# Kernel optimization log

Measured on AMD Instinct MI355X. Metric: run time of the kernel, lower is better.

## Reference

```python
import jax, jax.numpy as jnp
import numpy as np


def setup_inputs() -> dict:
    key = jax.random.key(0)
    k1, k2 = jax.random.split(key)
    inputs = jax.random.normal(k1, (32, 4096, 64), dtype=jnp.float32)
    embed = jax.random.normal(k2, (64, 1024), dtype=jnp.float32)  # [embed_dim, n_embed]
    return {"inputs": inputs, "embed": embed}


def reference(inputs, embed):
    # Eval-mode forward of VectorQuantizer (self.training == False, no EMA update).
    embed_dim, n_embed = embed.shape
    flat = inputs.reshape(-1, embed_dim)  # [N, D]
    # distances[n, k] = ||flat_n||^2 - 2 flat_n . e_k + ||e_k||^2
    distances = (
        jnp.sum(flat * flat, axis=1, keepdims=True)
        - 2.0 * (flat @ embed)
        + jnp.sum(embed * embed, axis=0, keepdims=True)
    )  # [N, n_embed]
    # torch.argmax(-distances, 1) == argmin(distances, 1) (same first-occurrence tie-break)
    encoding_indices = jnp.argmin(distances, axis=1)  # [N] int
    idx = encoding_indices.reshape(inputs.shape[:-1])  # [B, T]
    # quantize: F.embedding(idx, embed.T) -> gather rows of embed.T
    quantized = jnp.take(embed.T, idx, axis=0)  # [B, T, D]
    codes = jnp.concatenate([inputs, quantized], axis=-1)  # [B, T, 2D]
    # straight-through estimator
    quantized_st = inputs + jax.lax.stop_gradient(quantized - inputs)
    return quantized_st, codes, idx
```

## Files before the change

### kernel.cpp

```cpp
#include <hip/hip_runtime.h>

#define D 64
#define KCODES 1024
#define PTS_PER_BLK 256
#define MTILES 16
#define NT 4
#define CODE_CHUNKS 4
#define PTILES 512
#define WL_CAP 2048

typedef _Float16 f16x8 __attribute__((ext_vector_type(8)));
typedef float f32x4 __attribute__((ext_vector_type(4)));

static __device__ __forceinline__ unsigned short f2h(float f) {
  _Float16 h = (_Float16)f;
  return __builtin_bit_cast(unsigned short, h);
}

static __device__ __forceinline__ void evalExact(const float* __restrict__ inputs,
                                                 const float* __restrict__ embedT,
                                                 const float* __restrict__ en2,
                                                 const float* s_fn2,
                                                 int p0blk, int pl, int c,
                                                 unsigned long long* s_best) {
  int p = p0blk + pl;
  const float* f = inputs + (size_t)p * D;
  const float* e = embedT + (size_t)c * D;
  float a0 = 0.f, a1 = 0.f, a2 = 0.f, a3 = 0.f;
#pragma unroll
  for (int d = 0; d < D; d += 4) {
    a0 = fmaf(f[d + 0], e[d + 0], a0);
    a1 = fmaf(f[d + 1], e[d + 1], a1);
    a2 = fmaf(f[d + 2], e[d + 2], a2);
    a3 = fmaf(f[d + 3], e[d + 3], a3);
  }
  float dot = (a0 + a1) + (a2 + a3);
  float dist = fmaf(-2.f, dot, s_fn2[pl]) + en2[c];
  unsigned long long key = ((unsigned long long)__float_as_uint(dist) << 32) | (unsigned)c;
  atomicMin(&s_best[pl], key);
}

__global__ void __launch_bounds__(256) vq_prep(const float* __restrict__ embed,
                                               const float* __restrict__ inputs,
                                               float* __restrict__ embedT,
                                               unsigned short* __restrict__ embedTh,
                                               float* __restrict__ en2,
                                               int* __restrict__ en2max_bits,
                                               float* __restrict__ fn2,
                                               unsigned long long* __restrict__ best) {
  const int bid = blockIdx.x;
  const int tid = threadIdx.x;
  if (bid < KCODES / 256) {
    int k = bid * 256 + tid;
    float row[D];
    float s = 0.f;
#pragma unroll
    for (int d = 0; d < D; ++d) {
      float e = embed[d * KCODES + k];
      row[d] = e;
      s = fmaf(e, e, s);
    }
    en2[k] = s;
    float4* o4 = reinterpret_cast<float4*>(embedT + (size_t)k * D);
#pragma unroll
    for (int j = 0; j < 16; ++j)
      o4[j] = make_float4(row[4 * j], row[4 * j + 1], row[4 * j + 2], row[4 * j + 3]);
    unsigned us[32];
#pragma unroll
    for (int j = 0; j < 32; ++j) {
      unsigned lo = f2h(row[2 * j]);
      unsigned hi = f2h(row[2 * j + 1]);
      us[j] = lo | (hi << 16);
    }
    uint4* ob = reinterpret_cast<uint4*>(embedTh + (size_t)k * D);
#pragma unroll
    for (int j = 0; j < 8; ++j)
      ob[j] = make_uint4(us[4 * j], us[4 * j + 1], us[4 * j + 2], us[4 * j + 3]);
    float m = s;
#pragma unroll
    for (int off = 32; off; off >>= 1) m = fmaxf(m, __shfl_down(m, off, 64));
    if ((tid & 63) == 0) atomicMax(en2max_bits, __float_as_int(m));
  } else {
    int p = (bid - KCODES / 256) * 256 + tid;
    const float4* i4 = reinterpret_cast<const float4*>(inputs + (size_t)p * D);
    float s = 0.f;
#pragma unroll
    for (int j = 0; j < 16; ++j) {
      float4 v = i4[j];
      s = fmaf(v.x, v.x, s); s = fmaf(v.y, v.y, s);
      s = fmaf(v.z, v.z, s); s = fmaf(v.w, v.w, s);
    }
    fn2[p] = s;
    best[p] = ~0ull;
  }
}

__global__ void __launch_bounds__(256, 4) vq_partial(
    const float* __restrict__ inputs, const float* __restrict__ embedT,
    const unsigned short* __restrict__ embedTh, const float* __restrict__ en2,
    const float* __restrict__ fn2, const int* __restrict__ en2max_bits,
    unsigned long long* __restrict__ best) {
  __shared__ unsigned long long s_best[PTS_PER_BLK];
  __shared__ unsigned s_wl[WL_CAP];
  __shared__ int s_wcount;
  __shared__ float s_fn2[PTS_PER_BLK];
  __shared__ float s_wmin[2][4][16];

  const int tid = threadIdx.x;
  const int w = tid >> 6;
  const int l = tid & 63;
  const int l15 = l & 15;
  const int lg = l >> 4;
  const int chunk = blockIdx.x / PTILES;
  const int ptile = blockIdx.x % PTILES;
  const int p0blk = ptile * PTS_PER_BLK;
  const int cb = chunk * 256 + w * 64;

  s_best[tid] = ~0ull;
  if (tid == 0) s_wcount = 0;
  s_fn2[tid] = fn2[p0blk + tid];

  const float en2max = __int_as_float(*en2max_bits);

  f16x8 bfr[NT][2];
  float en2v[NT];
#pragma unroll
  for (int t = 0; t < NT; ++t) {
    const f16x8* bp = reinterpret_cast<const f16x8*>(
        embedTh + (size_t)(cb + 16 * t + l15) * D + lg * 8);
    bfr[t][0] = bp[0];
    bfr[t][1] = bp[4];
    en2v[t] = en2[cb + 16 * t + l15];
  }

  __syncthreads();

#pragma unroll 1
  for (int mt = 0; mt < MTILES; ++mt) {
    const int p0 = p0blk + mt * 16;
    const float* arow = inputs + (size_t)(p0 + l15) * D + lg * 8;
    float4 a0 = *reinterpret_cast<const float4*>(arow + 0);
    float4 a1 = *reinterpret_cast<const float4*>(arow + 4);
    float4 a2 = *reinterpret_cast<const float4*>(arow + 32);
    float4 a3 = *reinterpret_cast<const float4*>(arow + 36);
    f16x8 af0, af1;
    af0[0] = (_Float16)a0.x; af0[1] = (_Float16)a0.y; af0[2] = (_Float16)a0.z; af0[3] = (_Float16)a0.w;
    af0[4] = (_Float16)a1.x; af0[5] = (_Float16)a1.y; af0[6] = (_Float16)a1.z; af0[7] = (_Float16)a1.w;
    af1[0] = (_Float16)a2.x; af1[1] = (_Float16)a2.y; af1[2] = (_Float16)a2.z; af1[3] = (_Float16)a2.w;
    af1[4] = (_Float16)a3.x; af1[5] = (_Float16)a3.y; af1[6] = (_Float16)a3.z; af1[7] = (_Float16)a3.w;

    f32x4 acc[NT];
#pragma unroll
    for (int t = 0; t < NT; ++t) acc[t] = (f32x4){0.f, 0.f, 0.f, 0.f};
#pragma unroll
    for (int t = 0; t < NT; ++t)
      acc[t] = __builtin_amdgcn_mfma_f32_16x16x32_f16(af0, bfr[t][0], acc[t], 0, 0, 0);
#pragma unroll
    for (int t = 0; t < NT; ++t)
      acc[t] = __builtin_amdgcn_mfma_f32_16x16x32_f16(af1, bfr[t][1], acc[t], 0, 0, 0);

#pragma unroll
    for (int t = 0; t < NT; ++t)
#pragma unroll
      for (int r = 0; r < 4; ++r)
        acc[t][r] = fmaf(-2.f, acc[t][r], en2v[t]);

    float m[4];
#pragma unroll
    for (int r = 0; r < 4; ++r) {
      float mm = acc[0][r];
#pragma unroll
      for (int t = 1; t < NT; ++t) mm = fminf(mm, acc[t][r]);
#pragma unroll
      for (int s = 1; s < 16; s <<= 1) mm = fminf(mm, __shfl_xor(mm, s, 16));
      m[r] = mm;
    }
    if (l15 == 0) {
#pragma unroll
      for (int r = 0; r < 4; ++r) s_wmin[mt & 1][w][lg * 4 + r] = m[r];
    }
    __syncthreads();
    float fnv[4];
#pragma unroll
    for (int r = 0; r < 4; ++r) fnv[r] = s_fn2[mt * 16 + lg * 4 + r];
    float thr[4];
#pragma unroll
    for (int r = 0; r < 4; ++r) {
      int q = lg * 4 + r;
      float fm = fminf(fminf(s_wmin[mt & 1][0][q], s_wmin[mt & 1][1][q]),
                       fminf(s_wmin[mt & 1][2][q], s_wmin[mt & 1][3][q]));
      thr[r] = fm + (0.00390625f * sqrtf(fnv[r] * en2max) + 0.01f);
    }
#pragma unroll
    for (int t = 0; t < NT; ++t)
#pragma unroll
      for (int r = 0; r < 4; ++r)
        if (acc[t][r] <= thr[r]) {
          int pl = mt * 16 + lg * 4 + r;
          int c = cb + 16 * t + l15;
          int pos = atomicAdd(&s_wcount, 1);
          if (pos < WL_CAP) s_wl[pos] = (unsigned)((pl << 10) | c);
          else evalExact(inputs, embedT, en2, s_fn2, p0blk, pl, c, s_best);
        }
  }

  __syncthreads();

  int wc = s_wcount; if (wc > WL_CAP) wc = WL_CAP;
  for (int i = tid; i < wc; i += 256)
    evalExact(inputs, embedT, en2, s_fn2, p0blk, (int)(s_wl[i] >> 10), (int)(s_wl[i] & 1023), s_best);
  __syncthreads();

  atomicMin(&best[p0blk + tid], s_best[tid]);
}

__global__ void __launch_bounds__(256) vq_finalize(
    const float* __restrict__ inputs, const float* __restrict__ embedT,
    const unsigned long long* __restrict__ best,
    float* __restrict__ out_q, float* __restrict__ out_codes,
    float* __restrict__ out_idx) {
  const int tid = threadIdx.x;
  const int p0blk = blockIdx.x * 256;
  const int sub = tid & 3;
#pragma unroll 1
  for (int pass = 0; pass < 4; ++pass) {
    int pl = pass * 64 + (tid >> 2);
    int p = p0blk + pl;
    unsigned long long key = best[p];
    int c = (int)(unsigned)(key & 0xFFFFFFFFu);
    const f32x4* qrow = reinterpret_cast<const f32x4*>(embedT + (size_t)c * D);
    const f32x4* frow = reinterpret_cast<const f32x4*>(inputs + (size_t)p * D);
    f32x4* oq = reinterpret_cast<f32x4*>(out_q + (size_t)p * D);
    f32x4* oc = reinterpret_cast<f32x4*>(out_codes + (size_t)p * 2 * D);
#pragma unroll
    for (int j = 0; j < 4; ++j) {
      int i4 = j * 4 + sub;
      f32x4 qv = qrow[i4];
      f32x4 fv = frow[i4];
      oq[i4] = qv;
      oc[i4] = fv;
      oc[16 + i4] = qv;
    }
    if (sub == 0) out_idx[p] = (float)c;
  }
}

extern "C" void kernel_launch(void* const* d_in, const int* in_sizes, int n_in,
                              void* d_out, int out_size, void* d_ws, size_t ws_size,
                              hipStream_t stream) {
  const float* inputs = (const float*)d_in[0];
  const float* embed  = (const float*)d_in[1];
  int N = in_sizes[0] / D;

  unsigned long long* best  = (unsigned long long*)d_ws;
  float* embedT             = (float*)(best + N);
  unsigned short* embedTh   = (unsigned short*)(embedT + KCODES * D);
  float* en2                = (float*)(embedTh + KCODES * D);
  float* fn2                = en2 + KCODES;
  int* en2max_bits          = (int*)(fn2 + N);

  float* out = (float*)d_out;
  float* out_q     = out;
  float* out_codes = out + (size_t)N * D;
  float* out_idx   = out + (size_t)N * D * 3;

  vq_prep<<<KCODES / 256 + N / 256, 256, 0, stream>>>(embed, inputs, embedT, embedTh,
                                                      en2, en2max_bits, fn2, best);
  vq_partial<<<CODE_CHUNKS * PTILES, 256, 0, stream>>>(inputs, embedT, embedTh, en2,
                                                       fn2, en2max_bits, best);
  vq_finalize<<<N / 256, 256, 0, stream>>>(inputs, embedT, best, out_q, out_codes, out_idx);
}
```

Before: 314.4 us.

## Drop per-tile block barrier via wave-local thresholds and deferred refinement; prefetch next A tile

Candidate filtering no longer waits on a block-wide barrier every M-tile. Each wave now filters against its own local minimum plus margin. Candidates are stored together with their approximate distance, and after the loop they are re-filtered against the block-wide threshold before exact evaluation. The input rows for the next tile are also loaded one iteration ahead to hide global load latency. The trade-offs are a larger shared worklist (64-bit entries), more candidates collected because wave-local thresholds are looser, and a higher chance of overflowing the worklist, which triggers inline exact evaluation.

New measurement: 379.9 us. 1.21x slower.

```diff
diff --git a/kernel.cpp b/kernel.cpp
--- a/kernel.cpp
+++ b/kernel.cpp
@@ -101,10 +101,11 @@
     const float* __restrict__ fn2, const int* __restrict__ en2max_bits,
     unsigned long long* __restrict__ best) {
   __shared__ unsigned long long s_best[PTS_PER_BLK];
-  __shared__ unsigned s_wl[WL_CAP];
+  __shared__ unsigned long long s_wl[WL_CAP];
   __shared__ int s_wcount;
   __shared__ float s_fn2[PTS_PER_BLK];
-  __shared__ float s_wmin[2][4][16];
+  __shared__ float s_pmin[4][PTS_PER_BLK];
+  __shared__ float s_thr[PTS_PER_BLK];
 
   const int tid = threadIdx.x;
   const int w = tid >> 6;
@@ -135,19 +136,29 @@
 
   __syncthreads();
 
+  float4 A0, A1, A2, A3;
+  {
+    const float* arow = inputs + (size_t)(p0blk + l15) * D + lg * 8;
+    A0 = *reinterpret_cast<const float4*>(arow + 0);
+    A1 = *reinterpret_cast<const float4*>(arow + 4);
+    A2 = *reinterpret_cast<const float4*>(arow + 32);
+    A3 = *reinterpret_cast<const float4*>(arow + 36);
+  }
+
 #pragma unroll 1
   for (int mt = 0; mt < MTILES; ++mt) {
-    const int p0 = p0blk + mt * 16;
-    const float* arow = inputs + (size_t)(p0 + l15) * D + lg * 8;
-    float4 a0 = *reinterpret_cast<const float4*>(arow + 0);
-    float4 a1 = *reinterpret_cast<const float4*>(arow + 4);
-    float4 a2 = *reinterpret_cast<const float4*>(arow + 32);
-    float4 a3 = *reinterpret_cast<const float4*>(arow + 36);
+    const int mtn = (mt + 1 < MTILES) ? mt + 1 : mt;
+    const float* an = inputs + (size_t)(p0blk + mtn * 16 + l15) * D + lg * 8;
+    float4 N0 = *reinterpret_cast<const float4*>(an + 0);
+    float4 N1 = *reinterpret_cast<const float4*>(an + 4);
+    float4 N2 = *reinterpret_cast<const float4*>(an + 32);
+    float4 N3 = *reinterpret_cast<const float4*>(an + 36);
+
     f16x8 af0, af1;
-    af0[0] = (_Float16)a0.x; af0[1] = (_Float16)a0.y; af0[2] = (_Float16)a0.z; af0[3] = (_Float16)a0.w;
-    af0[4] = (_Float16)a1.x; af0[5] = (_Float16)a1.y; af0[6] = (_Float16)a1.z; af0[7] = (_Float16)a1.w;
-    af1[0] = (_Float16)a2.x; af1[1] = (_Float16)a2.y; af1[2] = (_Float16)a2.z; af1[3] = (_Float16)a2.w;
-    af1[4] = (_Float16)a3.x; af1[5] = (_Float16)a3.y; af1[6] = (_Float16)a3.z; af1[7] = (_Float16)a3.w;
+    af0[0] = (_Float16)A0.x; af0[1] = (_Float16)A0.y; af0[2] = (_Float16)A0.z; af0[3] = (_Float16)A0.w;
+    af0[4] = (_Float16)A1.x; af0[5] = (_Float16)A1.y; af0[6] = (_Float16)A1.z; af0[7] = (_Float16)A1.w;
+    af1[0] = (_Float16)A2.x; af1[1] = (_Float16)A2.y; af1[2] = (_Float16)A2.z; af1[3] = (_Float16)A2.w;
+    af1[4] = (_Float16)A3.x; af1[5] = (_Float16)A3.y; af1[6] = (_Float16)A3.z; af1[7] = (_Float16)A3.w;
 
     f32x4 acc[NT];
 #pragma unroll
@@ -177,38 +188,50 @@
     }
     if (l15 == 0) {
 #pragma unroll
-      for (int r = 0; r < 4; ++r) s_wmin[mt & 1][w][lg * 4 + r] = m[r];
-    }
-    __syncthreads();
-    float fnv[4];
-#pragma unroll
-    for (int r = 0; r < 4; ++r) fnv[r] = s_fn2[mt * 16 + lg * 4 + r];
-    float thr[4];
+      for (int r = 0; r < 4; ++r) s_pmin[w][mt * 16 + lg * 4 + r] = m[r];
+    }
+    float fnv[4], thrw[4];
 #pragma unroll
     for (int r = 0; r < 4; ++r) {
-      int q = lg * 4 + r;
-      float fm = fminf(fminf(s_wmin[mt & 1][0][q], s_wmin[mt & 1][1][q]),
-                       fminf(s_wmin[mt & 1][2][q], s_wmin[mt & 1][3][q]));
-      thr[r] = fm + (0.00390625f * sqrtf(fnv[r] * en2max) + 0.01f);
+      fnv[r] = s_fn2[mt * 16 + lg * 4 + r];
+      thrw[r] = m[r] + (0.00390625f * sqrtf(fnv[r] * en2max) + 0.01f);
     }
 #pragma unroll
     for (int t = 0; t < NT; ++t)
 #pragma unroll
       for (int r = 0; r < 4; ++r)
-        if (acc[t][r] <= thr[r]) {
+        if (acc[t][r] <= thrw[r]) {
           int pl = mt * 16 + lg * 4 + r;
           int c = cb + 16 * t + l15;
           int pos = atomicAdd(&s_wcount, 1);
-          if (pos < WL_CAP) s_wl[pos] = (unsigned)((pl << 10) | c);
-          else evalExact(inputs, embedT, en2, s_fn2, p0blk, pl, c, s_best);
+          if (pos < WL_CAP)
+            s_wl[pos] = ((unsigned long long)__float_as_uint(acc[t][r]) << 32) |
+                        (unsigned)((pl << 10) | c);
+          else
+            evalExact(inputs, embedT, en2, s_fn2, p0blk, pl, c, s_best);
         }
-  }
-
+
+    A0 = N0; A1 = N1; A2 = N2; A3 = N3;
+  }
+
+  __syncthreads();
+
+  {
+    float fm = fminf(fminf(s_pmin[0][tid], s_pmin[1][tid]),
+                     fminf(s_pmin[2][tid], s_pmin[3][tid]));
+    s_thr[tid] = fm + (0.00390625f * sqrtf(s_fn2[tid] * en2max) + 0.01f);
+  }
   __syncthreads();
 
   int wc = s_wcount; if (wc > WL_CAP) wc = WL_CAP;
-  for (int i = tid; i < wc; i += 256)
-    evalExact(inputs, embedT, en2, s_fn2, p0blk, (int)(s_wl[i] >> 10), (int)(s_wl[i] & 1023), s_best);
+  for (int i = tid; i < wc; i += 256) {
+    unsigned long long e = s_wl[i];
+    float dv = __uint_as_float((unsigned)(e >> 32));
+    int pl = (int)((e >> 10) & 255);
+    int c = (int)(e & 1023);
+    if (dv <= s_thr[pl])
+      evalExact(inputs, embedT, en2, s_fn2, p0blk, pl, c, s_best);
+  }
   __syncthreads();
 
   atomicMin(&best[p0blk + tid], s_best[tid]);
```

## Fuse finalize into partial kernel via last-block-done counter per point tile

Applied to the files above, without the earlier changes.

Removes the separate finalize kernel. Each point tile now keeps a completion counter, and the last of the four code-chunk blocks to finish writes the quantized outputs, codes and indices. Block indices are remapped so that the four chunks of a tile (and groups of eight tiles) are scheduled close together, which should improve L2 reuse of the input rows. This saves one kernel launch and its tail, at the cost of threadfence and atomic overhead plus uneven work across blocks.

Measured after the change: 524.5 us. 66.9% more time.

```diff
diff --git a/kernel.cpp b/kernel.cpp
--- a/kernel.cpp
+++ b/kernel.cpp
@@ -47,7 +47,8 @@
                                                float* __restrict__ en2,
                                                int* __restrict__ en2max_bits,
                                                float* __restrict__ fn2,
-                                               unsigned long long* __restrict__ best) {
+                                               unsigned long long* __restrict__ best,
+                                               int* __restrict__ done) {
   const int bid = blockIdx.x;
   const int tid = threadIdx.x;
   if (bid < KCODES / 256) {
@@ -92,6 +93,7 @@
     }
     fn2[p] = s;
     best[p] = ~0ull;
+    if (tid == 0) done[bid - KCODES / 256] = 0;
   }
 }
 
@@ -99,20 +101,24 @@
     const float* __restrict__ inputs, const float* __restrict__ embedT,
     const unsigned short* __restrict__ embedTh, const float* __restrict__ en2,
     const float* __restrict__ fn2, const int* __restrict__ en2max_bits,
-    unsigned long long* __restrict__ best) {
+    unsigned long long* __restrict__ best, int* __restrict__ done,
+    float* __restrict__ out_q, float* __restrict__ out_codes,
+    float* __restrict__ out_idx) {
   __shared__ unsigned long long s_best[PTS_PER_BLK];
   __shared__ unsigned s_wl[WL_CAP];
   __shared__ int s_wcount;
   __shared__ float s_fn2[PTS_PER_BLK];
   __shared__ float s_wmin[2][4][16];
+  __shared__ int s_last;
 
   const int tid = threadIdx.x;
   const int w = tid >> 6;
   const int l = tid & 63;
   const int l15 = l & 15;
   const int lg = l >> 4;
-  const int chunk = blockIdx.x / PTILES;
-  const int ptile = blockIdx.x % PTILES;
+  const int bid = blockIdx.x;
+  const int ptile = (bid >> 5) * 8 + (bid & 7);
+  const int chunk = (bid >> 3) & 3;
   const int p0blk = ptile * PTS_PER_BLK;
   const int cb = chunk * 256 + w * 64;
 
@@ -212,36 +218,34 @@
   __syncthreads();
 
   atomicMin(&best[p0blk + tid], s_best[tid]);
-}
-
-__global__ void __launch_bounds__(256) vq_finalize(
-    const float* __restrict__ inputs, const float* __restrict__ embedT,
-    const unsigned long long* __restrict__ best,
-    float* __restrict__ out_q, float* __restrict__ out_codes,
-    float* __restrict__ out_idx) {
-  const int tid = threadIdx.x;
-  const int p0blk = blockIdx.x * 256;
-  const int sub = tid & 3;
+  __threadfence();
+  __syncthreads();
+  if (tid == 0) s_last = (atomicAdd(&done[ptile], 1) == CODE_CHUNKS - 1);
+  __syncthreads();
+
+  if (s_last) {
+    const int sub = tid & 3;
 #pragma unroll 1
-  for (int pass = 0; pass < 4; ++pass) {
-    int pl = pass * 64 + (tid >> 2);
-    int p = p0blk + pl;
-    unsigned long long key = best[p];
-    int c = (int)(unsigned)(key & 0xFFFFFFFFu);
-    const f32x4* qrow = reinterpret_cast<const f32x4*>(embedT + (size_t)c * D);
-    const f32x4* frow = reinterpret_cast<const f32x4*>(inputs + (size_t)p * D);
-    f32x4* oq = reinterpret_cast<f32x4*>(out_q + (size_t)p * D);
-    f32x4* oc = reinterpret_cast<f32x4*>(out_codes + (size_t)p * 2 * D);
-#pragma unroll
-    for (int j = 0; j < 4; ++j) {
-      int i4 = j * 4 + sub;
-      f32x4 qv = qrow[i4];
-      f32x4 fv = frow[i4];
-      oq[i4] = qv;
-      oc[i4] = fv;
-      oc[16 + i4] = qv;
-    }
-    if (sub == 0) out_idx[p] = (float)c;
+    for (int pass = 0; pass < 4; ++pass) {
+      int pl = pass * 64 + (tid >> 2);
+      int p = p0blk + pl;
+      unsigned long long key = atomicMin(&best[p], ~0ull);
+      int c = (int)(unsigned)(key & 0xFFFFFFFFu);
+      const f32x4* qrow = reinterpret_cast<const f32x4*>(embedT + (size_t)c * D);
+      const f32x4* frow = reinterpret_cast<const f32x4*>(inputs + (size_t)p * D);
+      f32x4* oq = reinterpret_cast<f32x4*>(out_q + (size_t)p * D);
+      f32x4* oc = reinterpret_cast<f32x4*>(out_codes + (size_t)p * 2 * D);
+#pragma unroll
+      for (int j = 0; j < 4; ++j) {
+        int i4 = j * 4 + sub;
+        f32x4 qv = qrow[i4];
+        f32x4 fv = frow[i4];
+        oq[i4] = qv;
+        oc[i4] = fv;
+        oc[16 + i4] = qv;
+      }
+      if (sub == 0) out_idx[p] = (float)c;
+    }
   }
 }
 
@@ -258,6 +262,7 @@
   float* en2                = (float*)(embedTh + KCODES * D);
   float* fn2                = en2 + KCODES;
   int* en2max_bits          = (int*)(fn2 + N);
+  int* done                 = en2max_bits + 1;
 
   float* out = (float*)d_out;
   float* out_q     = out;
@@ -265,8 +270,8 @@
   float* out_idx   = out + (size_t)N * D * 3;
 
   vq_prep<<<KCODES / 256 + N / 256, 256, 0, stream>>>(embed, inputs, embedT, embedTh,
-                                                      en2, en2max_bits, fn2, best);
+                                                      en2, en2max_bits, fn2, best, done);
   vq_partial<<<CODE_CHUNKS * PTILES, 256, 0, stream>>>(inputs, embedT, embedTh, en2,
-                                                       fn2, en2max_bits, best);
-  vq_finalize<<<N / 256, 256, 0, stream>>>(inputs, embedT, best, out_q, out_codes, out_idx);
-}
+                                                       fn2, en2max_bits, best, done,
+                                                       out_q, out_codes, out_idx);
+}
```
